# Performance work log

Measured on AMD Instinct MI355X. Metric: run time of the kernel, lower is better.

## Reference

```python
import jax, jax.numpy as jnp
import numpy as np
import math

PH, PW = 14, 14      # patch size
DH, DW = 3, 3        # DCT block size
BINS = 256


def _dct_matrix(size: int) -> np.ndarray:
    m = np.zeros((size, size), dtype=np.float32)
    for i in range(size):
        for j in range(size):
            if i == 0:
                m[i, j] = math.sqrt(1.0 / size)
            else:
                m[i, j] = math.sqrt(2.0 / size) * math.cos(math.pi * (2 * j + 1) * i / (2 * size))
    return m


def setup_inputs() -> dict:
    key = jax.random.key(0)
    x = jax.random.uniform(key, (16, 3, 448, 448), dtype=jnp.float32)
    dct_matrix = jnp.asarray(_dct_matrix(DH))
    return {"x": x, "dct_matrix": dct_matrix}


def reference(x, dct_matrix):
    B, C, H, W = x.shape
    Hp, Wp = H // PH, W // PW
    # extract non-overlapping patches -> (B, Hp, Wp, C, PH, PW)
    patches = x.reshape(B, C, Hp, PH, Wp, PW).transpose(0, 2, 4, 1, 3, 5)

    # ---- per-patch pixel-value entropy (histogram via scatter-add) ----
    N = PH * PW
    pi = jnp.clip(jnp.round(jax.lax.stop_gradient(patches) * 255.0), 0, 255).astype(jnp.int32)
    flat = pi.reshape(-1, N)                       # (P, N), P = B*Hp*Wp*C
    P = flat.shape[0]
    counts = jnp.zeros((P, BINS), jnp.float32).at[jnp.arange(P)[:, None], flat].add(1.0)
    prob = counts / N + 1e-10
    entropy = -(prob * jnp.log2(prob)).sum(-1).reshape(B, Hp, Wp, C)

    # ---- sliding 3x3 windows inside each patch (stride 1) ----
    n = PH - DH + 1                                # 12 window positions per axis
    wins = jnp.stack(
        [patches[..., di:di + n, dj:dj + n] for di in range(DH) for dj in range(DW)],
        axis=-1,
    ).reshape(B, Hp, Wp, C, n, n, DH, DW)          # last two dims = within-window offsets

    # 2D DCT: D @ block @ D^T
    dct = jnp.einsum('ij,...jk,lk->...il', dct_matrix, wins, dct_matrix)

    # ---- direction variance of normalized stds ----
    S1 = jnp.std(dct, axis=-1).mean(-1)                       # rows
    S2 = jnp.std(dct, axis=-2).mean(-1)                       # cols
    S3 = jnp.std(jnp.diagonal(dct, axis1=-2, axis2=-1), axis=-1)
    S4 = jnp.std(jnp.diagonal(jnp.flip(dct, axis=-1), axis1=-2, axis2=-1), axis=-1)
    S = (S1 + S2 + S3 + S4) / 4.0 + 1e-8
    psi = jnp.var(jnp.stack([S1 / S, S2 / S, S3 / S, S4 / S], axis=-1), axis=-1, ddof=1)
    psi_m = psi.mean(axis=(-1, -2))                           # (B, Hp, Wp, C)

    richness = psi_m * entropy
    return richness.mean(-1)                                  # (B, Hp, Wp)
```

## Files before the change

### kernel.cpp

```cpp
#include <hip/hip_runtime.h>
#include <math.h>


typedef unsigned int uint32;

__device__ __forceinline__ float fsqrt_fast(float x) { return __builtin_amdgcn_sqrtf(x); }
__device__ __forceinline__ float frcp_fast(float x)  { return __builtin_amdgcn_rcpf(x);  }
__device__ __forceinline__ float flog2_fast(float x) { return __builtin_amdgcn_logf(x);  }

__device__ __forceinline__ float std3_fast(float a, float b, float c) {
    float s = a + b + c;
    float q = fmaf(a, a, fmaf(b, b, c * c));
    float v = fmaf(q, (1.0f / 3.0f), (s * s) * (-1.0f / 9.0f));
    return fsqrt_fast(fmaxf(v, 0.0f));
}

__global__ __launch_bounds__(192, 8) void richness_kernel(
    const float* __restrict__ x,
    const float* __restrict__ dctm,
    float* __restrict__ out)
{
    const int bid = blockIdx.x;
    const int wpg = bid & 3;
    const int hp  = (bid >> 2) & 31;
    const int b   = bid >> 7;
    const int tid = threadIdx.x;

    __shared__ uint32 hist[6][256];
    __shared__ float  psiPart[24][24];
    __shared__ float  entAcc[24];
    __shared__ float  richAcc[24];

    const float k0 = dctm[0];
    const float k1 = dctm[3];
    const float k2 = dctm[6];

    for (int i = tid; i < 6 * 256; i += 192) ((uint32*)hist)[i] = 0u;
    __syncthreads();

    for (int t = tid; t < 1176; t += 192) {
        int ch  = t / 392;
        int rem = t - ch * 392;
        int row = rem / 28;
        int col = (rem - row * 28) * 4;
        const float* src = x + (((size_t)(b * 3 + ch) * 448 + hp * 14 + row) * 448) + wpg * 112 + col;
        float4 v = *reinterpret_cast<const float4*>(src);
#pragma unroll
        for (int e = 0; e < 4; ++e) {
            float val = (&v.x)[e];
            int bin = (int)rintf(val * 255.0f);
            bin = min(max(bin, 0), 255);
            int ce = col + e;
            int p  = (ce * 2341) >> 15;
            int pc = ch * 8 + p;
            atomicAdd(&hist[pc >> 2][bin], 1u << ((pc & 3) * 8));
        }
    }

#pragma unroll
    for (int kr = 0; kr < 3; ++kr) {
        int rho  = tid + 192 * kr;
        int pc   = rho / 24;
        int rr   = rho - pc * 24;
        int ch   = pc >> 3, p = pc & 7;
        int wi   = rr >> 1, half = rr & 1;
        const float* base = x + (((size_t)(b * 3 + ch) * 448 + hp * 14 + wi) * 448)
                              + wpg * 112 + p * 14 + half * 6;

        float r0[8], r1[8], r2[8];
#pragma unroll
        for (int c2 = 0; c2 < 4; ++c2) {
            float2 a = *reinterpret_cast<const float2*>(base + c2 * 2);
            float2 bbv = *reinterpret_cast<const float2*>(base + 448 + c2 * 2);
            float2 cv = *reinterpret_cast<const float2*>(base + 896 + c2 * 2);
            r0[c2 * 2] = a.x;  r0[c2 * 2 + 1] = a.y;
            r1[c2 * 2] = bbv.x; r1[c2 * 2 + 1] = bbv.y;
            r2[c2 * 2] = cv.x; r2[c2 * 2 + 1] = cv.y;
        }

        float t0[8], t1[8], t2[8];
#pragma unroll
        for (int J = 0; J < 8; ++J) {
            float s = r0[J] + r2[J];
            t0[J] = k0 * (s + r1[J]);
            t1[J] = k1 * (r0[J] - r2[J]);
            t2[J] = k2 * fmaf(-2.0f, r1[J], s);
        }

        float psi_run = 0.0f;
#pragma unroll
        for (int j = 0; j < 6; ++j) {
            float X0 = t0[j],     X1 = t1[j],     X2 = t2[j];
            float Y0 = t0[j + 1], Y1 = t1[j + 1], Y2 = t2[j + 1];
            float Z0 = t0[j + 2], Z1 = t1[j + 2], Z2 = t2[j + 2];
            float xz0 = X0 + Z0, xz1 = X1 + Z1, xz2 = X2 + Z2;
            float d00 = k0 * (xz0 + Y0), d01 = k1 * (X0 - Z0), d02 = k2 * fmaf(-2.0f, Y0, xz0);
            float d10 = k0 * (xz1 + Y1), d11 = k1 * (X1 - Z1), d12 = k2 * fmaf(-2.0f, Y1, xz1);
            float d20 = k0 * (xz2 + Y2), d21 = k1 * (X2 - Z2), d22 = k2 * fmaf(-2.0f, Y2, xz2);

            float S1 = (std3_fast(d00, d01, d02) + std3_fast(d10, d11, d12) + std3_fast(d20, d21, d22)) * (1.0f / 3.0f);
            float S2 = (std3_fast(d00, d10, d20) + std3_fast(d01, d11, d21) + std3_fast(d02, d12, d22)) * (1.0f / 3.0f);
            float S3 = std3_fast(d00, d11, d22);
            float S4 = std3_fast(d02, d11, d20);

            float sumS = (S1 + S2) + (S3 + S4);
            float sumQ = fmaf(S1, S1, fmaf(S2, S2, fmaf(S3, S3, S4 * S4)));
            float h    = fmaxf(fmaf(-0.25f * sumS, sumS, sumQ), 0.0f);
            float Sm   = fmaf(sumS, 0.25f, 1e-8f);
            float inv  = frcp_fast(Sm);
            psi_run    = fmaf(h * inv * inv, (1.0f / 3.0f), psi_run);
        }
        psiPart[pc][rr] = psi_run;
    }
    __syncthreads();

    {
        const int pcE = tid >> 3, sub = tid & 7;
        const int rowW = pcE >> 2, sh = (pcE & 3) * 8;
        float negent = 0.0f;
#pragma unroll
        for (int kk = 0; kk < 32; ++kk) {
            uint32 c = (hist[rowW][sub + 8 * kk] >> sh) & 0xffu;
            float pr = (float)c * (1.0f / 196.0f) + 1e-10f;
            negent = fmaf(pr, flog2_fast(pr), negent);
        }
#pragma unroll
        for (int off = 1; off < 8; off <<= 1) negent += __shfl_xor(negent, off, 64);
        if (sub == 0) entAcc[pcE] = -negent;
    }
    __syncthreads();

    if (tid < 24) {
        float s = 0.0f;
#pragma unroll
        for (int r = 0; r < 24; ++r) s += psiPart[tid][r];
        richAcc[tid] = (s * (1.0f / 144.0f)) * entAcc[tid];
    }
    __syncthreads();

    if (tid < 8) {
        float r = (richAcc[tid] + richAcc[8 + tid] + richAcc[16 + tid]) * (1.0f / 3.0f);
        out[(b * 32 + hp) * 32 + wpg * 8 + tid] = r;
    }
}

extern "C" void kernel_launch(void* const* d_in, const int* in_sizes, int n_in,
                              void* d_out, int out_size, void* d_ws, size_t ws_size,
                              hipStream_t stream) {
    const float* x    = (const float*)d_in[0];
    const float* dctm = (const float*)d_in[1];
    float* out        = (float*)d_out;

    richness_kernel<<<2048, 192, 0, stream>>>(x, dctm, out);
}
```

Before: 38.60 us.

## Halve patches per block and reduce psi with wavefront shuffles

```diff
diff --git a/kernel.cpp b/kernel.cpp
--- a/kernel.cpp
+++ b/kernel.cpp
@@ -21,29 +21,27 @@
     float* __restrict__ out)
 {
     const int bid = blockIdx.x;
-    const int wpg = bid & 3;
-    const int hp  = (bid >> 2) & 31;
-    const int b   = bid >> 7;
+    const int wpg = bid & 7;
+    const int hp  = (bid >> 3) & 31;
+    const int b   = bid >> 8;
     const int tid = threadIdx.x;
 
-    __shared__ uint32 hist[6][256];
-    __shared__ float  psiPart[24][24];
-    __shared__ float  entAcc[24];
-    __shared__ float  richAcc[24];
+    __shared__ uint32 hist[3][256];
+    __shared__ float  richAcc[12];
 
     const float k0 = dctm[0];
     const float k1 = dctm[3];
     const float k2 = dctm[6];
 
-    for (int i = tid; i < 6 * 256; i += 192) ((uint32*)hist)[i] = 0u;
+    for (int i = tid; i < 768; i += 192) ((uint32*)hist)[i] = 0u;
     __syncthreads();
 
-    for (int t = tid; t < 1176; t += 192) {
-        int ch  = t / 392;
-        int rem = t - ch * 392;
-        int row = rem / 28;
-        int col = (rem - row * 28) * 4;
-        const float* src = x + (((size_t)(b * 3 + ch) * 448 + hp * 14 + row) * 448) + wpg * 112 + col;
+    for (int t = tid; t < 588; t += 192) {
+        int chh = t / 196;
+        int rem = t - chh * 196;
+        int row = rem / 14;
+        int col = (rem - row * 14) * 4;
+        const float* src = x + (((size_t)(b * 3 + chh) * 448 + hp * 14 + row) * 448) + wpg * 56 + col;
         float4 v = *reinterpret_cast<const float4*>(src);
 #pragma unroll
         for (int e = 0; e < 4; ++e) {
@@ -52,47 +50,40 @@
             bin = min(max(bin, 0), 255);
             int ce = col + e;
             int p  = (ce * 2341) >> 15;
-            int pc = ch * 8 + p;
-            atomicAdd(&hist[pc >> 2][bin], 1u << ((pc & 3) * 8));
+            atomicAdd(&hist[chh][bin], 1u << (p * 8));
         }
     }
 
+    const int pc = tid >> 4;
+    const int s  = tid & 15;
+    const int ch = pc >> 2, p = pc & 3;
+
+    float psi3 = 0.0f;
 #pragma unroll
-    for (int kr = 0; kr < 3; ++kr) {
-        int rho  = tid + 192 * kr;
-        int pc   = rho / 24;
-        int rr   = rho - pc * 24;
-        int ch   = pc >> 3, p = pc & 7;
-        int wi   = rr >> 1, half = rr & 1;
+    for (int kq = 0; kq < 3; ++kq) {
+        int r  = s + 16 * kq;
+        int wi = r >> 2;
+        int j0 = (r & 3) * 3;
         const float* base = x + (((size_t)(b * 3 + ch) * 448 + hp * 14 + wi) * 448)
-                              + wpg * 112 + p * 14 + half * 6;
+                              + wpg * 56 + p * 14 + j0;
 
-        float r0[8], r1[8], r2[8];
+        float t0[5], t1[5], t2[5];
 #pragma unroll
-        for (int c2 = 0; c2 < 4; ++c2) {
-            float2 a = *reinterpret_cast<const float2*>(base + c2 * 2);
-            float2 bbv = *reinterpret_cast<const float2*>(base + 448 + c2 * 2);
-            float2 cv = *reinterpret_cast<const float2*>(base + 896 + c2 * 2);
-            r0[c2 * 2] = a.x;  r0[c2 * 2 + 1] = a.y;
-            r1[c2 * 2] = bbv.x; r1[c2 * 2 + 1] = bbv.y;
-            r2[c2 * 2] = cv.x; r2[c2 * 2 + 1] = cv.y;
+        for (int c = 0; c < 5; ++c) {
+            float a  = base[c];
+            float bb = base[448 + c];
+            float cv = base[896 + c];
+            float ss = a + cv;
+            t0[c] = k0 * (ss + bb);
+            t1[c] = k1 * (a - cv);
+            t2[c] = k2 * fmaf(-2.0f, bb, ss);
         }
 
-        float t0[8], t1[8], t2[8];
 #pragma unroll
-        for (int J = 0; J < 8; ++J) {
-            float s = r0[J] + r2[J];
-            t0[J] = k0 * (s + r1[J]);
-            t1[J] = k1 * (r0[J] - r2[J]);
-            t2[J] = k2 * fmaf(-2.0f, r1[J], s);
-        }
-
-        float psi_run = 0.0f;
-#pragma unroll
-        for (int j = 0; j < 6; ++j) {
-            float X0 = t0[j],     X1 = t1[j],     X2 = t2[j];
-            float Y0 = t0[j + 1], Y1 = t1[j + 1], Y2 = t2[j + 1];
-            float Z0 = t0[j + 2], Z1 = t1[j + 2], Z2 = t2[j + 2];
+        for (int m = 0; m < 3; ++m) {
+            float X0 = t0[m],     X1 = t1[m],     X2 = t2[m];
+            float Y0 = t0[m + 1], Y1 = t1[m + 1], Y2 = t2[m + 1];
+            float Z0 = t0[m + 2], Z1 = t1[m + 2], Z2 = t2[m + 2];
             float xz0 = X0 + Z0, xz1 = X1 + Z1, xz2 = X2 + Z2;
             float d00 = k0 * (xz0 + Y0), d01 = k1 * (X0 - Z0), d02 = k2 * fmaf(-2.0f, Y0, xz0);
             float d10 = k0 * (xz1 + Y1), d11 = k1 * (X1 - Z1), d12 = k2 * fmaf(-2.0f, Y1, xz1);
@@ -108,39 +99,33 @@
             float h    = fmaxf(fmaf(-0.25f * sumS, sumS, sumQ), 0.0f);
             float Sm   = fmaf(sumS, 0.25f, 1e-8f);
             float inv  = frcp_fast(Sm);
-            psi_run    = fmaf(h * inv * inv, (1.0f / 3.0f), psi_run);
+            psi3       = fmaf(h * inv * inv, (1.0f / 3.0f), psi3);
         }
-        psiPart[pc][rr] = psi_run;
     }
+
+#pragma unroll
+    for (int off = 1; off < 16; off <<= 1) psi3 += __shfl_xor(psi3, off, 64);
+
     __syncthreads();
 
     {
-        const int pcE = tid >> 3, sub = tid & 7;
-        const int rowW = pcE >> 2, sh = (pcE & 3) * 8;
         float negent = 0.0f;
+        const int sh = p * 8;
 #pragma unroll
-        for (int kk = 0; kk < 32; ++kk) {
-            uint32 c = (hist[rowW][sub + 8 * kk] >> sh) & 0xffu;
+        for (int kk = 0; kk < 16; ++kk) {
+            uint32 c = (hist[ch][s + 16 * kk] >> sh) & 0xffu;
             float pr = (float)c * (1.0f / 196.0f) + 1e-10f;
             negent = fmaf(pr, flog2_fast(pr), negent);
         }
 #pragma unroll
-        for (int off = 1; off < 8; off <<= 1) negent += __shfl_xor(negent, off, 64);
-        if (sub == 0) entAcc[pcE] = -negent;
+        for (int off = 1; off < 16; off <<= 1) negent += __shfl_xor(negent, off, 64);
+        if (s == 0) richAcc[pc] = (psi3 * (1.0f / 144.0f)) * (-negent);
     }
     __syncthreads();
 
-    if (tid < 24) {
-        float s = 0.0f;
-#pragma unroll
-        for (int r = 0; r < 24; ++r) s += psiPart[tid][r];
-        richAcc[tid] = (s * (1.0f / 144.0f)) * entAcc[tid];
-    }
-    __syncthreads();
-
-    if (tid < 8) {
-        float r = (richAcc[tid] + richAcc[8 + tid] + richAcc[16 + tid]) * (1.0f / 3.0f);
-        out[(b * 32 + hp) * 32 + wpg * 8 + tid] = r;
+    if (tid < 4) {
+        float rv = (richAcc[tid] + richAcc[4 + tid] + richAcc[8 + tid]) * (1.0f / 3.0f);
+        out[(b * 32 + hp) * 32 + wpg * 4 + tid] = rv;
     }
 }
 
@@ -151,5 +136,5 @@
     const float* dctm = (const float*)d_in[1];
     float* out        = (float*)d_out;
 
-    richness_kernel<<<2048, 192, 0, stream>>>(x, dctm, out);
+    richness_kernel<<<4096, 192, 0, stream>>>(x, dctm, out);
 }
```

Result: slower. 40.54 us (+5.0%).
